# Optimization experiments

Hardware: AMD Instinct MI355X
Metric: run time of the kernel (lower is better)

Reference implementation:

```python
import jax, jax.numpy as jnp
import numpy as np

N = 50000        # nodes
E = 800000       # edges (before self-loops)
IN_DIM = 128
HID = 32         # per-head hidden channels, conv1
OUT = 32         # per-head output channels, conv2
H = 4            # attention heads
NEG_SLOPE = 0.2  # PyG GATConv default


def setup_inputs() -> dict:
    key = jax.random.key(0)
    ks = jax.random.split(key, 12)
    x = jax.random.normal(ks[0], (N, IN_DIM), dtype=jnp.float32)
    edge_index = jax.random.randint(ks[1], (2, E), 0, N, dtype=jnp.int32)
    s = 0.05
    W1 = jax.random.normal(ks[2], (IN_DIM, H * HID), dtype=jnp.float32) * s
    a_src1 = jax.random.normal(ks[3], (H, HID), dtype=jnp.float32) * s
    a_dst1 = jax.random.normal(ks[4], (H, HID), dtype=jnp.float32) * s
    b1 = jnp.zeros((H * HID,), dtype=jnp.float32)
    W2 = jax.random.normal(ks[5], (H * HID, H * OUT), dtype=jnp.float32) * s
    a_src2 = jax.random.normal(ks[6], (H, OUT), dtype=jnp.float32) * s
    a_dst2 = jax.random.normal(ks[7], (H, OUT), dtype=jnp.float32) * s
    b2 = jnp.zeros((H * OUT,), dtype=jnp.float32)
    return {"x": x, "edge_index": edge_index,
            "W1": W1, "a_src1": a_src1, "a_dst1": a_dst1, "b1": b1,
            "W2": W2, "a_src2": a_src2, "a_dst2": a_dst2, "b2": b2}


def _gat_conv(x, src, dst, W, a_src, a_dst, b, heads, ch):
    # linear transform: [N, heads, ch]
    h = (x @ W).reshape(-1, heads, ch)
    # per-node attention logits [N, heads]
    al_src = jnp.einsum('nhc,hc->nh', h, a_src)
    al_dst = jnp.einsum('nhc,hc->nh', h, a_dst)
    # per-edge logits, leaky relu  [Etot, heads]
    e = jax.nn.leaky_relu(al_src[src] + al_dst[dst], negative_slope=NEG_SLOPE)
    # softmax over incoming edges of each destination node
    m = jax.lax.stop_gradient(jax.ops.segment_max(e, dst, num_segments=N))
    ex = jnp.exp(e - m[dst])
    denom = jax.ops.segment_sum(ex, dst, num_segments=N)
    alpha = ex / denom[dst]                      # [Etot, heads]
    # weighted scatter-aggregate of source features
    out = jax.ops.segment_sum(alpha[:, :, None] * h[src], dst, num_segments=N)
    return out.reshape(N, heads * ch) + b


def reference(x, edge_index, W1, a_src1, a_dst1, b1, W2, a_src2, a_dst2, b2):
    # PyG GATConv add_self_loops=True
    loops = jnp.arange(N, dtype=edge_index.dtype)
    src = jnp.concatenate([edge_index[0], loops])
    dst = jnp.concatenate([edge_index[1], loops])
    # eval mode: dropout is identity
    h = _gat_conv(x, src, dst, W1, a_src1, a_dst1, b1, H, HID)
    h = jax.nn.elu(h)
    out = _gat_conv(h, src, dst, W2, a_src2, a_dst2, b2, H, OUT)
    return out
```

## Files before the change

kernel.cpp:

```cpp
#include <hip/hip_runtime.h>
#include <hip/hip_bf16.h>

#define NN 50000
#define EE 800000
#define ETOT (EE + NN)
#define F 128
#define HEADS 4
#define RPB 128
#define NB ((NN + 1023) / 1024)

typedef __bf16 bf16x8 __attribute__((ext_vector_type(8)));
typedef float  f32x4  __attribute__((ext_vector_type(4)));

__device__ __forceinline__ unsigned short f32_to_bf16(float f) {
    unsigned int u = __float_as_uint(f);
    u += 0x7fffu + ((u >> 16) & 1u);
    return (unsigned short)(u >> 16);
}
__device__ __forceinline__ float bf16bits_to_f32(unsigned short s) {
    return __uint_as_float(((unsigned int)s) << 16);
}
__device__ __forceinline__ float bflo(unsigned int u) { return __uint_as_float(u << 16); }
__device__ __forceinline__ float bfhi(unsigned int u) { return __uint_as_float(u & 0xffff0000u); }

union BU { unsigned short u[8]; bf16x8 v; };


__global__ void wpack_k(const float* __restrict__ W1, const float* __restrict__ W2,
                        unsigned short* __restrict__ wf) {
    int t = blockIdx.x * blockDim.x + threadIdx.x;
    if (t >= 2 * 2048) return;
    int which = t >> 11;
    int rem = t & 2047;
    int lane = rem & 63;
    int tile = rem >> 6;
    int kt = tile >> 3, nt = tile & 7;
    int q = lane >> 4, c = lane & 15;
    const float* W = which ? W2 : W1;
    BU vh, vl;
#pragma unroll
    for (int j = 0; j < 8; j++) {
        float w = W[(kt * 32 + q * 8 + j) * F + nt * 16 + c];
        unsigned short hb = f32_to_bf16(w);
        vh.u[j] = hb;
        vl.u[j] = f32_to_bf16(w - bf16bits_to_f32(hb));
    }
    size_t base_h = ((size_t)(which * 2 + 0) * 2048 + tile * 64 + lane) * 8;
    size_t base_l = ((size_t)(which * 2 + 1) * 2048 + tile * 64 + lane) * 8;
    *(bf16x8*)&wf[base_h] = vh.v;
    *(bf16x8*)&wf[base_l] = vl.v;
}


__launch_bounds__(512, 4)
__global__ void gemm_mfma(const float* __restrict__ A, const unsigned short* __restrict__ wf,
                          const float* __restrict__ a_src, const float* __restrict__ a_dst,
                          unsigned short* __restrict__ Cb, float* __restrict__ als,
                          float* __restrict__ ald, int M,
                          const int* __restrict__ ei, int* __restrict__ counts,
                          int* __restrict__ pos, int gemm_blocks) {
    __shared__ unsigned char smem[65536];
    int tid = threadIdx.x;
    int w = tid >> 6, lane = tid & 63;
    int m = lane & 15, q = lane >> 4;
    int row0 = blockIdx.x * RPB + w * 16;

    {
        const uint4* src = (const uint4*)wf;
        uint4* dst = (uint4*)smem;
#pragma unroll
        for (int i = 0; i < 8; i++) dst[tid + i * 512] = src[tid + i * 512];
    }

    int ar = row0 + m; if (ar >= M) ar = 0;
    const float* arow = A + (size_t)ar * F + q * 8;
    float4 a0[4], a1[4];
#pragma unroll
    for (int kt = 0; kt < 4; kt++) {
        a0[kt] = *(const float4*)(arow + kt * 32);
        a1[kt] = *(const float4*)(arow + kt * 32 + 4);
    }
    __syncthreads();

    const unsigned short* lds_h = (const unsigned short*)smem;
    const unsigned short* lds_l = (const unsigned short*)(smem + 32768);

    f32x4 acc[8];
#pragma unroll
    for (int nt = 0; nt < 8; nt++) acc[nt] = (f32x4){0.f, 0.f, 0.f, 0.f};

#pragma unroll
    for (int kt = 0; kt < 4; kt++) {
        float av[8] = {a0[kt].x, a0[kt].y, a0[kt].z, a0[kt].w,
                       a1[kt].x, a1[kt].y, a1[kt].z, a1[kt].w};
        BU ah, al;
#pragma unroll
        for (int j = 0; j < 8; j++) {
            unsigned short hb = f32_to_bf16(av[j]);
            ah.u[j] = hb;
            al.u[j] = f32_to_bf16(av[j] - bf16bits_to_f32(hb));
        }
#pragma unroll
        for (int nt = 0; nt < 8; nt++) {
            int bo = ((kt * 8 + nt) * 64 + lane) * 8;
            bf16x8 bh = *(const bf16x8*)&lds_h[bo];
            bf16x8 bl = *(const bf16x8*)&lds_l[bo];
            acc[nt] = __builtin_amdgcn_mfma_f32_16x16x32_bf16(ah.v, bh, acc[nt], 0, 0, 0);
            acc[nt] = __builtin_amdgcn_mfma_f32_16x16x32_bf16(al.v, bh, acc[nt], 0, 0, 0);
            acc[nt] = __builtin_amdgcn_mfma_f32_16x16x32_bf16(ah.v, bl, acc[nt], 0, 0, 0);
        }
    }
    __syncthreads();

    int rr = lane >> 2;
    int head = lane & 3;
    int c0 = head * 32;
    int gr = row0 + rr;
    for (int phase = 0; phase < 2; phase++) {
        if ((w >> 2) == phase) {
            float* L = (float*)smem + (w & 3) * (16 * 132);
#pragma unroll
            for (int nt = 0; nt < 8; nt++)
#pragma unroll
                for (int r = 0; r < 4; r++)
                    L[(q * 4 + r) * 132 + nt * 16 + m] = acc[nt][r];
            float v[32];
#pragma unroll
            for (int i = 0; i < 8; i++)
                *(float4*)&v[i * 4] = *(const float4*)&L[rr * 132 + c0 + i * 4];
            if (gr < M) {
#pragma unroll
                for (int i = 0; i < 4; i++) {
                    uint4 pk;
                    pk.x = (unsigned)f32_to_bf16(v[i * 8 + 0]) | ((unsigned)f32_to_bf16(v[i * 8 + 1]) << 16);
                    pk.y = (unsigned)f32_to_bf16(v[i * 8 + 2]) | ((unsigned)f32_to_bf16(v[i * 8 + 3]) << 16);
                    pk.z = (unsigned)f32_to_bf16(v[i * 8 + 4]) | ((unsigned)f32_to_bf16(v[i * 8 + 5]) << 16);
                    pk.w = (unsigned)f32_to_bf16(v[i * 8 + 6]) | ((unsigned)f32_to_bf16(v[i * 8 + 7]) << 16);
                    *(uint4*)&Cb[(size_t)gr * F + c0 + i * 8] = pk;
                }
                float ps = 0.f, pd = 0.f;
#pragma unroll
                for (int i = 0; i < 32; i++) {
                    ps += v[i] * a_src[c0 + i];
                    pd += v[i] * a_dst[c0 + i];
                }
                als[gr * HEADS + head] = ps;
                ald[gr * HEADS + head] = pd;
            }
        }
        __syncthreads();
    }

    if (ei) {
        int stride = gemm_blocks * 512;
        for (int e = blockIdx.x * 512 + tid; e < ETOT; e += stride) {
            int dst = (e < EE) ? ei[EE + e] : (e - EE);
            pos[e] = atomicAdd(&counts[dst], 1);
        }
    }
}


__launch_bounds__(1024)
__global__ void scan_block_k(const int* __restrict__ counts, int* __restrict__ row_ptr,
                             int* __restrict__ bsum, int n) {
    int tid = threadIdx.x;
    int i = blockIdx.x * 1024 + tid;
    int v = (i < n) ? counts[i] : 0;
    int lane = tid & 63;
    int wave = tid >> 6;
    int x = v;
#pragma unroll
    for (int off = 1; off < 64; off <<= 1) {
        int t = __shfl_up(x, off, 64);
        if (lane >= off) x += t;
    }
    __shared__ int wsum[16];
    if (lane == 63) wsum[wave] = x;
    __syncthreads();
    if (wave == 0) {
        int w = (lane < 16) ? wsum[lane] : 0;
#pragma unroll
        for (int off = 1; off < 16; off <<= 1) {
            int t = __shfl_up(w, off, 64);
            if (lane >= off) w += t;
        }
        if (lane < 16) wsum[lane] = w;
    }
    __syncthreads();
    int base = (wave > 0) ? wsum[wave - 1] : 0;
    int incl = base + x;
    if (i < n) row_ptr[i] = incl - v;
    if (tid == 1023) bsum[blockIdx.x] = incl;
}

__launch_bounds__(256)
__global__ void scan_add_k(int* __restrict__ row_ptr, const int* __restrict__ bsum, int n) {
    __shared__ int off_s[NB];
    if (threadIdx.x < 64) {
        int lane = threadIdx.x;
        int v = (lane < NB) ? bsum[lane] : 0;
        int x = v;
#pragma unroll
        for (int o = 1; o < 64; o <<= 1) {
            int t = __shfl_up(x, o, 64);
            if (lane >= o) x += t;
        }
        if (lane < NB) off_s[lane] = x - v;
    }
    __syncthreads();
    int i = blockIdx.x * blockDim.x + threadIdx.x;
    if (i < n) row_ptr[i] += off_s[i >> 10];
    if (i == 0) row_ptr[n] = ETOT;
}

__global__ void fill_k(const int* __restrict__ ei, const int* __restrict__ row_ptr,
                       const int* __restrict__ pos, int* __restrict__ csr_src) {
    int e = blockIdx.x * blockDim.x + threadIdx.x;
    if (e >= ETOT) return;
    int src, dst;
    if (e < EE) { src = ei[e]; dst = ei[EE + e]; }
    else        { src = e - EE; dst = e - EE; }
    csr_src[row_ptr[dst] + pos[e]] = src;
}


__launch_bounds__(256)
__global__ void aggregate(const unsigned short* __restrict__ hb, const float* __restrict__ als,
                          const float* __restrict__ ald, const int* __restrict__ row_ptr,
                          const int* __restrict__ csr_src, const float* __restrict__ bias,
                          float* __restrict__ out, int apply_elu) {
    int tid = threadIdx.x;
    int lane = tid & 63;
    int g  = lane >> 4;
    int cl = lane & 15;
    int n = blockIdx.x * 16 + (tid >> 6) * 4 + g;
    int head = cl >> 2;
    float aldv = ald[n * HEADS + head];
    int jb = row_ptr[n], je = row_ptr[n + 1];

    float acc[8];
#pragma unroll
    for (int i = 0; i < 8; i++) acc[i] = 0.f;
    float den = 0.f;

    int j = jb;
    for (; j + 3 < je; j += 4) {
        int s0 = csr_src[j];
        int s1 = csr_src[j + 1];
        int s2 = csr_src[j + 2];
        int s3 = csr_src[j + 3];
        float e0 = als[s0 * HEADS + head];
        float e1 = als[s1 * HEADS + head];
        float e2 = als[s2 * HEADS + head];
        float e3 = als[s3 * HEADS + head];
        uint4 r0 = *(const uint4*)&hb[(size_t)s0 * F + cl * 8];
        uint4 r1 = *(const uint4*)&hb[(size_t)s1 * F + cl * 8];
        uint4 r2 = *(const uint4*)&hb[(size_t)s2 * F + cl * 8];
        uint4 r3 = *(const uint4*)&hb[(size_t)s3 * F + cl * 8];
        e0 += aldv; e1 += aldv; e2 += aldv; e3 += aldv;
        e0 = (e0 > 0.f) ? e0 : 0.2f * e0;
        e1 = (e1 > 0.f) ? e1 : 0.2f * e1;
        e2 = (e2 > 0.f) ? e2 : 0.2f * e2;
        e3 = (e3 > 0.f) ? e3 : 0.2f * e3;
        float p0 = __expf(e0), p1 = __expf(e1), p2 = __expf(e2), p3 = __expf(e3);
        den += (p0 + p1) + (p2 + p3);
        acc[0] += p0 * bflo(r0.x); acc[1] += p0 * bfhi(r0.x);
        acc[2] += p0 * bflo(r0.y); acc[3] += p0 * bfhi(r0.y);
        acc[4] += p0 * bflo(r0.z); acc[5] += p0 * bfhi(r0.z);
        acc[6] += p0 * bflo(r0.w); acc[7] += p0 * bfhi(r0.w);
        acc[0] += p1 * bflo(r1.x); acc[1] += p1 * bfhi(r1.x);
        acc[2] += p1 * bflo(r1.y); acc[3] += p1 * bfhi(r1.y);
        acc[4] += p1 * bflo(r1.z); acc[5] += p1 * bfhi(r1.z);
        acc[6] += p1 * bflo(r1.w); acc[7] += p1 * bfhi(r1.w);
        acc[0] += p2 * bflo(r2.x); acc[1] += p2 * bfhi(r2.x);
        acc[2] += p2 * bflo(r2.y); acc[3] += p2 * bfhi(r2.y);
        acc[4] += p2 * bflo(r2.z); acc[5] += p2 * bfhi(r2.z);
        acc[6] += p2 * bflo(r2.w); acc[7] += p2 * bfhi(r2.w);
        acc[0] += p3 * bflo(r3.x); acc[1] += p3 * bfhi(r3.x);
        acc[2] += p3 * bflo(r3.y); acc[3] += p3 * bfhi(r3.y);
        acc[4] += p3 * bflo(r3.z); acc[5] += p3 * bfhi(r3.z);
        acc[6] += p3 * bflo(r3.w); acc[7] += p3 * bfhi(r3.w);
    }
    for (; j < je; j++) {
        int s = csr_src[j];
        float e = als[s * HEADS + head] + aldv;
        uint4 raw = *(const uint4*)&hb[(size_t)s * F + cl * 8];
        e = (e > 0.f) ? e : 0.2f * e;
        float p = __expf(e);
        den += p;
        acc[0] += p * bflo(raw.x); acc[1] += p * bfhi(raw.x);
        acc[2] += p * bflo(raw.y); acc[3] += p * bfhi(raw.y);
        acc[4] += p * bflo(raw.z); acc[5] += p * bfhi(raw.z);
        acc[6] += p * bflo(raw.w); acc[7] += p * bfhi(raw.w);
    }

    float inv = 1.f / den;
    float v[8];
#pragma unroll
    for (int i = 0; i < 8; i++) {
        v[i] = acc[i] * inv + bias[cl * 8 + i];
        if (apply_elu) v[i] = (v[i] > 0.f) ? v[i] : (__expf(v[i]) - 1.f);
    }
    float4* op = (float4*)&out[(size_t)n * F + cl * 8];
    op[0] = make_float4(v[0], v[1], v[2], v[3]);
    op[1] = make_float4(v[4], v[5], v[6], v[7]);
}


extern "C" void kernel_launch(void* const* d_in, const int* in_sizes, int n_in,
                              void* d_out, int out_size, void* d_ws, size_t ws_size,
                              hipStream_t stream) {
    const float* x   = (const float*)d_in[0];
    const int*   ei  = (const int*)d_in[1];
    const float* W1  = (const float*)d_in[2];
    const float* as1 = (const float*)d_in[3];
    const float* ad1 = (const float*)d_in[4];
    const float* b1  = (const float*)d_in[5];
    const float* W2  = (const float*)d_in[6];
    const float* as2 = (const float*)d_in[7];
    const float* ad2 = (const float*)d_in[8];
    const float* b2  = (const float*)d_in[9];
    float* out = (float*)d_out;

    char* ws = (char*)d_ws;
    size_t off = 0;
    auto alloc = [&](size_t bytes) {
        void* p = ws + off;
        off += (bytes + 255) & ~(size_t)255;
        return p;
    };
    unsigned short* hb = (unsigned short*)alloc((size_t)NN * F * 2);
    float* als     = (float*)alloc((size_t)NN * HEADS * 4);
    float* ald     = (float*)alloc((size_t)NN * HEADS * 4);
    int*   counts  = (int*)alloc((size_t)NN * 4);
    int*   row_ptr = (int*)alloc((size_t)(NN + 1) * 4);
    int*   bsum    = (int*)alloc((size_t)NB * 4);
    int*   csr_src = (int*)alloc((size_t)ETOT * 4);
    int*   pos     = (int*)alloc((size_t)ETOT * 4);
    unsigned short* wf = (unsigned short*)alloc((size_t)4 * 2048 * 8 * 2);

    int GG = (NN + RPB - 1) / RPB;
    int agg_grid = (NN + 15) / 16;

    (void)hipMemsetAsync(counts, 0, (size_t)NN * 4, stream);
    wpack_k<<<16, 256, 0, stream>>>(W1, W2, wf);

    gemm_mfma<<<GG, 512, 0, stream>>>(x, wf, as1, ad1, hb, als, ald, NN,
                                      ei, counts, pos, GG);
    scan_block_k<<<NB, 1024, 0, stream>>>(counts, row_ptr, bsum, NN);
    scan_add_k<<<(NN + 255) / 256, 256, 0, stream>>>(row_ptr, bsum, NN);
    fill_k<<<(ETOT + 255) / 256, 256, 0, stream>>>(ei, row_ptr, pos, csr_src);
    aggregate<<<agg_grid, 256, 0, stream>>>(hb, als, ald, row_ptr, csr_src, b1, out, 1);

    gemm_mfma<<<GG, 512, 0, stream>>>(out, wf + (size_t)2 * 2048 * 8, as2, ad2, hb, als, ald, NN,
                                      (const int*)nullptr, (int*)nullptr, (int*)nullptr, GG);
    aggregate<<<agg_grid, 256, 0, stream>>>(hb, als, ald, row_ptr, csr_src, b2, out, 0);
}
```

Measured before the change: 261.7 us.

## Fold scan-add into consumers, zero counts in wpack, shrink GEMM blocks

The separate scan_add kernel is removed. Each consumer (fill_k, aggregate) now rebuilds the per-chunk prefix offsets from bsum in shared memory and adds them when reading row_ptr. The counts memset moves into wpack_k. The GEMM drops from 512-thread, 128-row blocks to 256-thread, 64-row blocks, which removes the two-phase epilogue, and it prefetches A one k-tile ahead instead of loading it all up front. These changes save two launches, but every aggregate and fill block now repeats a small scan.

After: 259.2 us. Within noise of the previous version (-1.0%).

```diff
diff --git a/kernel.cpp b/kernel.cpp
--- a/kernel.cpp
+++ b/kernel.cpp
@@ -6,7 +6,6 @@
 #define ETOT (EE + NN)
 #define F 128
 #define HEADS 4
-#define RPB 128
 #define NB ((NN + 1023) / 1024)
 
 typedef __bf16 bf16x8 __attribute__((ext_vector_type(8)));
@@ -27,9 +26,9 @@
 
 
 __global__ void wpack_k(const float* __restrict__ W1, const float* __restrict__ W2,
-                        unsigned short* __restrict__ wf) {
+                        unsigned short* __restrict__ wf, int* __restrict__ counts) {
     int t = blockIdx.x * blockDim.x + threadIdx.x;
-    if (t >= 2 * 2048) return;
+    for (int i = t; i < NN; i += 4096) counts[i] = 0;
     int which = t >> 11;
     int rem = t & 2047;
     int lane = rem & 63;
@@ -52,7 +51,7 @@
 }
 
 
-__launch_bounds__(512, 4)
+__launch_bounds__(256)
 __global__ void gemm_mfma(const float* __restrict__ A, const unsigned short* __restrict__ wf,
                           const float* __restrict__ a_src, const float* __restrict__ a_dst,
                           unsigned short* __restrict__ Cb, float* __restrict__ als,
@@ -63,23 +62,19 @@
     int tid = threadIdx.x;
     int w = tid >> 6, lane = tid & 63;
     int m = lane & 15, q = lane >> 4;
-    int row0 = blockIdx.x * RPB + w * 16;
+    int row0 = blockIdx.x * 64 + w * 16;
 
     {
         const uint4* src = (const uint4*)wf;
         uint4* dst = (uint4*)smem;
 #pragma unroll
-        for (int i = 0; i < 8; i++) dst[tid + i * 512] = src[tid + i * 512];
+        for (int i = 0; i < 16; i++) dst[tid + i * 256] = src[tid + i * 256];
     }
 
     int ar = row0 + m; if (ar >= M) ar = 0;
     const float* arow = A + (size_t)ar * F + q * 8;
-    float4 a0[4], a1[4];
-#pragma unroll
-    for (int kt = 0; kt < 4; kt++) {
-        a0[kt] = *(const float4*)(arow + kt * 32);
-        a1[kt] = *(const float4*)(arow + kt * 32 + 4);
-    }
+    float4 a0 = *(const float4*)(arow);
+    float4 a1 = *(const float4*)(arow + 4);
     __syncthreads();
 
     const unsigned short* lds_h = (const unsigned short*)smem;
@@ -91,8 +86,12 @@
 
 #pragma unroll
     for (int kt = 0; kt < 4; kt++) {
-        float av[8] = {a0[kt].x, a0[kt].y, a0[kt].z, a0[kt].w,
-                       a1[kt].x, a1[kt].y, a1[kt].z, a1[kt].w};
+        float4 n0, n1;
+        if (kt < 3) {
+            n0 = *(const float4*)(arow + (kt + 1) * 32);
+            n1 = *(const float4*)(arow + (kt + 1) * 32 + 4);
+        }
+        float av[8] = {a0.x, a0.y, a0.z, a0.w, a1.x, a1.y, a1.z, a1.w};
         BU ah, al;
 #pragma unroll
         for (int j = 0; j < 8; j++) {
@@ -109,51 +108,49 @@
             acc[nt] = __builtin_amdgcn_mfma_f32_16x16x32_bf16(al.v, bh, acc[nt], 0, 0, 0);
             acc[nt] = __builtin_amdgcn_mfma_f32_16x16x32_bf16(ah.v, bl, acc[nt], 0, 0, 0);
         }
-    }
-    __syncthreads();
+        if (kt < 3) { a0 = n0; a1 = n1; }
+    }
+    __syncthreads();
+
+    float* L = (float*)smem + w * (16 * 132);
+#pragma unroll
+    for (int nt = 0; nt < 8; nt++)
+#pragma unroll
+        for (int r = 0; r < 4; r++)
+            L[(q * 4 + r) * 132 + nt * 16 + m] = acc[nt][r];
 
     int rr = lane >> 2;
     int head = lane & 3;
     int c0 = head * 32;
     int gr = row0 + rr;
-    for (int phase = 0; phase < 2; phase++) {
-        if ((w >> 2) == phase) {
-            float* L = (float*)smem + (w & 3) * (16 * 132);
-#pragma unroll
-            for (int nt = 0; nt < 8; nt++)
-#pragma unroll
-                for (int r = 0; r < 4; r++)
-                    L[(q * 4 + r) * 132 + nt * 16 + m] = acc[nt][r];
-            float v[32];
-#pragma unroll
-            for (int i = 0; i < 8; i++)
-                *(float4*)&v[i * 4] = *(const float4*)&L[rr * 132 + c0 + i * 4];
-            if (gr < M) {
-#pragma unroll
-                for (int i = 0; i < 4; i++) {
-                    uint4 pk;
-                    pk.x = (unsigned)f32_to_bf16(v[i * 8 + 0]) | ((unsigned)f32_to_bf16(v[i * 8 + 1]) << 16);
-                    pk.y = (unsigned)f32_to_bf16(v[i * 8 + 2]) | ((unsigned)f32_to_bf16(v[i * 8 + 3]) << 16);
-                    pk.z = (unsigned)f32_to_bf16(v[i * 8 + 4]) | ((unsigned)f32_to_bf16(v[i * 8 + 5]) << 16);
-                    pk.w = (unsigned)f32_to_bf16(v[i * 8 + 6]) | ((unsigned)f32_to_bf16(v[i * 8 + 7]) << 16);
-                    *(uint4*)&Cb[(size_t)gr * F + c0 + i * 8] = pk;
-                }
-                float ps = 0.f, pd = 0.f;
-#pragma unroll
-                for (int i = 0; i < 32; i++) {
-                    ps += v[i] * a_src[c0 + i];
-                    pd += v[i] * a_dst[c0 + i];
-                }
-                als[gr * HEADS + head] = ps;
-                ald[gr * HEADS + head] = pd;
-            }
-        }
-        __syncthreads();
+    float v[32];
+#pragma unroll
+    for (int i = 0; i < 8; i++)
+        *(float4*)&v[i * 4] = *(const float4*)&L[rr * 132 + c0 + i * 4];
+
+    if (gr < M) {
+#pragma unroll
+        for (int i = 0; i < 4; i++) {
+            uint4 pk;
+            pk.x = (unsigned)f32_to_bf16(v[i * 8 + 0]) | ((unsigned)f32_to_bf16(v[i * 8 + 1]) << 16);
+            pk.y = (unsigned)f32_to_bf16(v[i * 8 + 2]) | ((unsigned)f32_to_bf16(v[i * 8 + 3]) << 16);
+            pk.z = (unsigned)f32_to_bf16(v[i * 8 + 4]) | ((unsigned)f32_to_bf16(v[i * 8 + 5]) << 16);
+            pk.w = (unsigned)f32_to_bf16(v[i * 8 + 6]) | ((unsigned)f32_to_bf16(v[i * 8 + 7]) << 16);
+            *(uint4*)&Cb[(size_t)gr * F + c0 + i * 8] = pk;
+        }
+        float ps = 0.f, pd = 0.f;
+#pragma unroll
+        for (int i = 0; i < 32; i++) {
+            ps += v[i] * a_src[c0 + i];
+            pd += v[i] * a_dst[c0 + i];
+        }
+        als[gr * HEADS + head] = ps;
+        ald[gr * HEADS + head] = pd;
     }
 
     if (ei) {
-        int stride = gemm_blocks * 512;
-        for (int e = blockIdx.x * 512 + tid; e < ETOT; e += stride) {
+        int stride = gemm_blocks * 256;
+        for (int e = blockIdx.x * 256 + tid; e < ETOT; e += stride) {
             int dst = (e < EE) ? ei[EE + e] : (e - EE);
             pos[e] = atomicAdd(&counts[dst], 1);
         }
@@ -194,50 +191,53 @@
     if (tid == 1023) bsum[blockIdx.x] = incl;
 }
 
-__launch_bounds__(256)
-__global__ void scan_add_k(int* __restrict__ row_ptr, const int* __restrict__ bsum, int n) {
-    __shared__ int off_s[NB];
-    if (threadIdx.x < 64) {
-        int lane = threadIdx.x;
-        int v = (lane < NB) ? bsum[lane] : 0;
+__device__ __forceinline__ void chunk_offsets(const int* __restrict__ bsum, int* off_s,
+                                              int tid) {
+    if (tid < 64) {
+        int v = (tid < NB) ? bsum[tid] : 0;
         int x = v;
 #pragma unroll
         for (int o = 1; o < 64; o <<= 1) {
             int t = __shfl_up(x, o, 64);
-            if (lane >= o) x += t;
-        }
-        if (lane < NB) off_s[lane] = x - v;
-    }
-    __syncthreads();
-    int i = blockIdx.x * blockDim.x + threadIdx.x;
-    if (i < n) row_ptr[i] += off_s[i >> 10];
-    if (i == 0) row_ptr[n] = ETOT;
-}
-
+            if (tid >= o) x += t;
+        }
+        if (tid < NB) off_s[tid] = x - v;
+    }
+    __syncthreads();
+}
+
+__launch_bounds__(256)
 __global__ void fill_k(const int* __restrict__ ei, const int* __restrict__ row_ptr,
-                       const int* __restrict__ pos, int* __restrict__ csr_src) {
+                       const int* __restrict__ bsum, const int* __restrict__ pos,
+                       int* __restrict__ csr_src) {
+    __shared__ int off_s[NB];
+    chunk_offsets(bsum, off_s, threadIdx.x);
     int e = blockIdx.x * blockDim.x + threadIdx.x;
     if (e >= ETOT) return;
     int src, dst;
     if (e < EE) { src = ei[e]; dst = ei[EE + e]; }
     else        { src = e - EE; dst = e - EE; }
-    csr_src[row_ptr[dst] + pos[e]] = src;
+    csr_src[row_ptr[dst] + off_s[dst >> 10] + pos[e]] = src;
 }
 
 
 __launch_bounds__(256)
 __global__ void aggregate(const unsigned short* __restrict__ hb, const float* __restrict__ als,
                           const float* __restrict__ ald, const int* __restrict__ row_ptr,
-                          const int* __restrict__ csr_src, const float* __restrict__ bias,
+                          const int* __restrict__ bsum, const int* __restrict__ csr_src,
+                          const float* __restrict__ bias,
                           float* __restrict__ out, int apply_elu) {
+    __shared__ int off_s[NB];
     int tid = threadIdx.x;
+    chunk_offsets(bsum, off_s, tid);
     int lane = tid & 63;
     int g  = lane >> 4;
     int cl = lane & 15;
     int n = blockIdx.x * 16 + (tid >> 6) * 4 + g;
     int head = cl >> 2;
     float aldv = ald[n * HEADS + head];
-    int jb = row_ptr[n], je = row_ptr[n + 1];
+    int jb = row_ptr[n] + off_s[n >> 10];
+    int je = (n + 1 < NN) ? (row_ptr[n + 1] + off_s[(n + 1) >> 10]) : ETOT;
 
     float acc[8];
 #pragma unroll
@@ -340,20 +340,18 @@
     int*   pos     = (int*)alloc((size_t)ETOT * 4);
     unsigned short* wf = (unsigned short*)alloc((size_t)4 * 2048 * 8 * 2);
 
-    int GG = (NN + RPB - 1) / RPB;
+    int GG = (NN + 63) / 64;
     int agg_grid = (NN + 15) / 16;
 
-    (void)hipMemsetAsync(counts, 0, (size_t)NN * 4, stream);
-    wpack_k<<<16, 256, 0, stream>>>(W1, W2, wf);
-
-    gemm_mfma<<<GG, 512, 0, stream>>>(x, wf, as1, ad1, hb, als, ald, NN,
+    wpack_k<<<16, 256, 0, stream>>>(W1, W2, wf, counts);
+
+    gemm_mfma<<<GG, 256, 0, stream>>>(x, wf, as1, ad1, hb, als, ald, NN,
                                       ei, counts, pos, GG);
     scan_block_k<<<NB, 1024, 0, stream>>>(counts, row_ptr, bsum, NN);
-    scan_add_k<<<(NN + 255) / 256, 256, 0, stream>>>(row_ptr, bsum, NN);
-    fill_k<<<(ETOT + 255) / 256, 256, 0, stream>>>(ei, row_ptr, pos, csr_src);
-    aggregate<<<agg_grid, 256, 0, stream>>>(hb, als, ald, row_ptr, csr_src, b1, out, 1);
-
-    gemm_mfma<<<GG, 512, 0, stream>>>(out, wf + (size_t)2 * 2048 * 8, as2, ad2, hb, als, ald, NN,
+    fill_k<<<(ETOT + 255) / 256, 256, 0, stream>>>(ei, row_ptr, bsum, pos, csr_src);
+    aggregate<<<agg_grid, 256, 0, stream>>>(hb, als, ald, row_ptr, bsum, csr_src, b1, out, 1);
+
+    gemm_mfma<<<GG, 256, 0, stream>>>(out, wf + (size_t)2 * 2048 * 8, as2, ad2, hb, als, ald, NN,
                                       (const int*)nullptr, (int*)nullptr, (int*)nullptr, GG);
-    aggregate<<<agg_grid, 256, 0, stream>>>(hb, als, ald, row_ptr, csr_src, b2, out, 0);
-}
+    aggregate<<<agg_grid, 256, 0, stream>>>(hb, als, ald, row_ptr, bsum, csr_src, b2, out, 0);
+}
```
